# Optimization experiments

Hardware: AMD Instinct MI355X
Metric: run time of the kernel (lower is better)

## Reference

```python
import jax, jax.numpy as jnp
import numpy as np

K = 128
HEADS = 8
B = 4
T = 2048


def setup_inputs() -> dict:
    key = jax.random.key(0)
    ks = jax.random.split(key, 6)
    x = jax.random.normal(ks[0], (B, T, K), dtype=jnp.float32)
    s = 1.0 / np.sqrt(K)
    # torch nn.Linear weights are (out_features, in_features)
    Wq = jax.random.uniform(ks[1], (HEADS * K, K), dtype=jnp.float32, minval=-s, maxval=s)
    Wk = jax.random.uniform(ks[2], (HEADS * K, K), dtype=jnp.float32, minval=-s, maxval=s)
    Wv = jax.random.uniform(ks[3], (HEADS * K, K), dtype=jnp.float32, minval=-s, maxval=s)
    su = 1.0 / np.sqrt(HEADS * K)
    Wu = jax.random.uniform(ks[4], (K, HEADS * K), dtype=jnp.float32, minval=-su, maxval=su)
    bu = jax.random.uniform(ks[5], (K,), dtype=jnp.float32, minval=-su, maxval=su)
    return {"x": x, "Wq": Wq, "Wk": Wk, "Wv": Wv, "Wu": Wu, "bu": bu}


def reference(x, Wq, Wk, Wv, Wu, bu):
    b, t, k = x.shape
    h = HEADS
    # project: Linear(k, k*h) then view(b,t,h,k); weight reshaped to (h, k_out, k_in)
    q = jnp.einsum('btk,hdk->bhtd', x, Wq.reshape(h, k, k))
    kk = jnp.einsum('btk,hdk->bhtd', x, Wk.reshape(h, k, k))
    v = jnp.einsum('btk,hdk->bhtd', x, Wv.reshape(h, k, k))
    scale = jnp.asarray(k, x.dtype) ** 0.25
    q = q / scale
    kk = kk / scale
    dot = jnp.einsum('bhtd,bhsd->bhts', q, kk)  # [b,h,t,t]
    att = jax.nn.softmax(dot, axis=-1)
    out = jnp.einsum('bhts,bhsd->bhtd', att, v)  # [b,h,t,k]
    out = out.transpose(0, 2, 1, 3).reshape(b, t, h * k)
    return out @ Wu.T + bu
```

## Files before the change

### kernel.cpp

```cpp
#include <hip/hip_runtime.h>
#include <cmath>

namespace {

constexpr int HEADS = 8;
constexpr int Bn = 4;
constexpr int Tn = 2048;
constexpr int Dn = 128;
constexpr float Q_PRESCALE = 0.1275174340f;

typedef _Float16 half8 __attribute__((ext_vector_type(8)));
typedef _Float16 half4 __attribute__((ext_vector_type(4)));
typedef _Float16 half2v __attribute__((ext_vector_type(2)));
typedef float f32x4 __attribute__((ext_vector_type(4)));
typedef float f32x16 __attribute__((ext_vector_type(16)));
typedef unsigned int u32;
typedef unsigned int u32x4 __attribute__((ext_vector_type(4)));

__global__ __launch_bounds__(256) void cast_kernel(
    const float* __restrict__ x, const float* __restrict__ Wq, const float* __restrict__ Wk,
    const float* __restrict__ Wv, const float* __restrict__ Wu, _Float16* __restrict__ xh,
    _Float16* __restrict__ WH) {
  const int idx = blockIdx.x * 256 + threadIdx.x;
  const size_t base = (size_t)idx * 8;
  const float* src;
  _Float16* dst;
  if (base < 1048576) {
    src = x + base;
    dst = xh + base;
  } else {
    const size_t r = base - 1048576;
    const int s = (int)(r >> 17);
    src = ((s == 0) ? Wq : (s == 1) ? Wk : (s == 2) ? Wv : Wu) + (r & 131071);
    dst = WH + r;
  }
  const float4 a = *reinterpret_cast<const float4*>(src);
  const float4 b = *reinterpret_cast<const float4*>(src + 4);
  half8 h;
  h[0] = (_Float16)a.x; h[1] = (_Float16)a.y; h[2] = (_Float16)a.z; h[3] = (_Float16)a.w;
  h[4] = (_Float16)b.x; h[5] = (_Float16)b.y; h[6] = (_Float16)b.z; h[7] = (_Float16)b.w;
  *reinterpret_cast<half8*>(dst) = h;
}

__global__ __launch_bounds__(256, 4) void proj_kernel(const _Float16* __restrict__ xh,
                                                      const _Float16* __restrict__ WH,
                                                      _Float16* __restrict__ Qh,
                                                      _Float16* __restrict__ Kh,
                                                      _Float16* __restrict__ Vt) {
  __shared__ _Float16 sB[128 * 136];
  const int tid = threadIdx.x;
  const int w = tid >> 6, lane = tid & 63, quad = lane >> 4, l16 = lane & 15;
  const int m0 = blockIdx.x * 128;
  const int n0 = blockIdx.y * 128;

#pragma unroll
  for (int it = 0; it < 8; ++it) {
    const int fid = tid + it * 256;
    const int r = fid >> 4, g = fid & 15;
    const half8 v = *reinterpret_cast<const half8*>(WH + (size_t)(n0 + r) * 128 + g * 8);
    const int p = g ^ (r & 15);
    *reinterpret_cast<half8*>(sB + r * 128 + p * 8) = v;
  }

  half8 af[2][4];
  const _Float16* xp = xh + (size_t)(m0 + w * 32 + l16) * 128 + quad * 8;
#pragma unroll
  for (int mt = 0; mt < 2; ++mt)
#pragma unroll
    for (int kk = 0; kk < 4; ++kk)
      af[mt][kk] = *reinterpret_cast<const half8*>(xp + mt * 16 * 128 + kk * 32);

  __syncthreads();

  f32x4 acc[2][8];
#pragma unroll
  for (int mt = 0; mt < 2; ++mt)
#pragma unroll
    for (int nt = 0; nt < 8; ++nt) acc[mt][nt] = (f32x4){0.f, 0.f, 0.f, 0.f};

#pragma unroll
  for (int kk = 0; kk < 4; ++kk)
#pragma unroll
    for (int nt = 0; nt < 8; ++nt) {
      const int r = nt * 16 + l16;
      const int p = (kk * 4 + quad) ^ l16;
      const half8 bf = *reinterpret_cast<const half8*>(sB + r * 128 + p * 8);
      acc[0][nt] = __builtin_amdgcn_mfma_f32_16x16x32_f16(af[0][kk], bf, acc[0][nt], 0, 0, 0);
      acc[1][nt] = __builtin_amdgcn_mfma_f32_16x16x32_f16(af[1][kk], bf, acc[1][nt], 0, 0, 0);
    }

  const int sel = n0 >> 10;
  const int h = (n0 >> 7) & 7;
  const int b = m0 >> 11;
  const int t0b = m0 & 2047;
  const int bh = b * HEADS + h;
  const float scale = (sel == 0) ? Q_PRESCALE : 1.0f;

  __syncthreads();

  if (sel < 2) {
#pragma unroll
    for (int mt = 0; mt < 2; ++mt)
#pragma unroll
      for (int nt = 0; nt < 8; ++nt)
#pragma unroll
        for (int r = 0; r < 4; ++r)
          sB[(w * 32 + mt * 16 + quad * 4 + r) * 136 + nt * 16 + l16] =
              (_Float16)(acc[mt][nt][r] * scale);
  } else {
#pragma unroll
    for (int mt = 0; mt < 2; ++mt)
#pragma unroll
      for (int nt = 0; nt < 8; ++nt)
#pragma unroll
        for (int r = 0; r < 4; ++r)
          sB[(nt * 16 + l16) * 136 + w * 32 + mt * 16 + quad * 4 + r] = (_Float16)acc[mt][nt][r];
  }
  __syncthreads();

  _Float16* dstbase;
  size_t rstride;
  if (sel == 0) {
    dstbase = Qh + ((size_t)bh * Tn + t0b) * Dn;
    rstride = Dn;
  } else if (sel == 1) {
    dstbase = Kh + ((size_t)bh * Tn + t0b) * Dn;
    rstride = Dn;
  } else {
    dstbase = Vt + ((size_t)bh * Dn) * Tn + t0b;
    rstride = Tn;
  }
#pragma unroll
  for (int it = 0; it < 8; ++it) {
    const int fid = tid + it * 256;
    const int r = fid >> 4, g = fid & 15;
    const half8 v = *reinterpret_cast<const half8*>(sB + r * 136 + g * 8);
    *reinterpret_cast<half8*>(dstbase + (size_t)r * rstride + g * 8) = v;
  }
}

__global__ __launch_bounds__(256, 1) void flash_kernel(const _Float16* __restrict__ Qh,
                                                       const _Float16* __restrict__ Kh,
                                                       const _Float16* __restrict__ Vt,
                                                       _Float16* __restrict__ Obh) {
  __shared__ _Float16 sAll[40960];

  const int tid = threadIdx.x;
  const int w = tid >> 6;
  const int lane = tid & 63;
  const int l31 = lane & 31;
  const int h = lane >> 5;
  const int qt = blockIdx.x;
  const int bh = blockIdx.y;
  constexpr int NT = Tn / 64;

  half8 qf[2][8];
#pragma unroll
  for (int qb = 0; qb < 2; ++qb) {
    const _Float16* Qp =
        Qh + ((size_t)bh * Tn + qt * 256 + w * 64 + qb * 32 + l31) * Dn + h * 8;
#pragma unroll
    for (int ds = 0; ds < 8; ++ds) qf[qb][ds] = *reinterpret_cast<const half8*>(Qp + ds * 16);
  }

  const _Float16* Kp = Kh + (size_t)bh * Tn * Dn;
  const _Float16* Vp = Vt + (size_t)bh * Dn * Tn;

  f32x16 o[4][2];
#pragma unroll
  for (int db = 0; db < 4; ++db)
#pragma unroll
    for (int qb = 0; qb < 2; ++qb) o[db][qb] = (f32x16)(0.f);
  float lsum[2] = {0.f, 0.f};

  half8 kreg[4], vreg[4];
  const int kr = tid >> 4, kg = tid & 15;
  const int vr = tid >> 3, vg = tid & 7;
  const int vG = (vg >> 1) * 2;
  const int vO = (vg & 1) * 4;

#pragma unroll
  for (int it = 0; it < 4; ++it) {
    kreg[it] = *reinterpret_cast<const half8*>(Kp + (size_t)(kr + it * 16) * Dn + kg * 8);
    vreg[it] = *reinterpret_cast<const half8*>(Vp + (size_t)(vr + it * 32) * Tn + vg * 8);
  }
  {
    _Float16* sK0 = sAll;
    _Float16* sV0 = sAll + 16384;
#pragma unroll
    for (int it = 0; it < 4; ++it) {
      const int r = kr + it * 16;
      const int p = kg ^ (r & 15);
      *reinterpret_cast<half8*>(sK0 + r * 128 + p * 8) = kreg[it];
      const int rv = vr + it * 32;
      const int sw = (rv & 7) ^ ((rv >> 1) & 4);
      const half8 v = vreg[it];
      half4 lo, hi;
      lo[0] = v[0]; lo[1] = v[1]; lo[2] = v[2]; lo[3] = v[3];
      hi[0] = v[4]; hi[1] = v[5]; hi[2] = v[6]; hi[3] = v[7];
      *reinterpret_cast<half4*>(sV0 + rv * 64 + ((vG ^ sw) * 8) + vO) = lo;
      *reinterpret_cast<half4*>(sV0 + rv * 64 + (((vG + 1) ^ sw) * 8) + vO) = hi;
    }
  }
#pragma unroll
  for (int it = 0; it < 4; ++it) {
    kreg[it] = *reinterpret_cast<const half8*>(Kp + (size_t)(64 + kr + it * 16) * Dn + kg * 8);
    vreg[it] = *reinterpret_cast<const half8*>(Vp + (size_t)(vr + it * 32) * Tn + 64 + vg * 8);
  }
  __syncthreads();

  f32x16 scA[2][2], scB[2][2];
#pragma unroll
  for (int a = 0; a < 2; ++a)
#pragma unroll
    for (int b2 = 0; b2 < 2; ++b2) scA[a][b2] = (f32x16)(0.f);
#pragma unroll
  for (int ds = 0; ds < 8; ++ds) {
    const int p = (ds * 2 + h) ^ (l31 & 15);
    const half8 kf0 = *reinterpret_cast<const half8*>(sAll + l31 * 128 + p * 8);
    const half8 kf1 = *reinterpret_cast<const half8*>(sAll + (32 + l31) * 128 + p * 8);
    scA[0][0] = __builtin_amdgcn_mfma_f32_32x32x16_f16(kf0, qf[0][ds], scA[0][0], 0, 0, 0);
    scA[0][1] = __builtin_amdgcn_mfma_f32_32x32x16_f16(kf1, qf[0][ds], scA[0][1], 0, 0, 0);
    scA[1][0] = __builtin_amdgcn_mfma_f32_32x32x16_f16(kf0, qf[1][ds], scA[1][0], 0, 0, 0);
    scA[1][1] = __builtin_amdgcn_mfma_f32_32x32x16_f16(kf1, qf[1][ds], scA[1][1], 0, 0, 0);
  }

  auto step = [&](int t, f32x16 (&sc)[2][2], f32x16 (&sn)[2][2]) {
    _Float16* sKn = sAll + ((t + 1) & 1) * 8192;
    _Float16* sVc = sAll + 16384 + (t % 3) * 8192;
    _Float16* sVn = sAll + 16384 + ((t + 1) % 3) * 8192;

    if (t + 1 < NT) {
#pragma unroll
      for (int it = 0; it < 4; ++it) {
        const int r = kr + it * 16;
        const int p = kg ^ (r & 15);
        *reinterpret_cast<half8*>(sKn + r * 128 + p * 8) = kreg[it];
        const int rv = vr + it * 32;
        const int sw = (rv & 7) ^ ((rv >> 1) & 4);
        const half8 v = vreg[it];
        half4 lo, hi;
        lo[0] = v[0]; lo[1] = v[1]; lo[2] = v[2]; lo[3] = v[3];
        hi[0] = v[4]; hi[1] = v[5]; hi[2] = v[6]; hi[3] = v[7];
        *reinterpret_cast<half4*>(sVn + rv * 64 + ((vG ^ sw) * 8) + vO) = lo;
        *reinterpret_cast<half4*>(sVn + rv * 64 + (((vG + 1) ^ sw) * 8) + vO) = hi;
      }
    }
    __syncthreads();
    if (t + 2 < NT) {
      const _Float16* knext = Kp + (size_t)(t + 2) * 64 * Dn;
      const _Float16* vnext = Vp + (t + 2) * 64;
#pragma unroll
      for (int it = 0; it < 4; ++it) {
        kreg[it] = *reinterpret_cast<const half8*>(knext + (size_t)(kr + it * 16) * Dn + kg * 8);
        vreg[it] = *reinterpret_cast<const half8*>(vnext + (size_t)(vr + it * 32) * Tn + vg * 8);
      }
    }

    if (t + 1 < NT) {
#pragma unroll
      for (int a = 0; a < 2; ++a)
#pragma unroll
        for (int b2 = 0; b2 < 2; ++b2) sn[a][b2] = (f32x16)(0.f);
    }

    half8 bfr[2][4];
#pragma unroll
    for (int i = 0; i < 4; ++i) {
      const int qb = i & 1, kb = i >> 1;
      {
        u32 pk[8];
        float part = 0.f;
#pragma unroll
        for (int j = 0; j < 8; ++j) {
          const float e0 = __builtin_amdgcn_exp2f(sc[qb][kb][2 * j]);
          const float e1 = __builtin_amdgcn_exp2f(sc[qb][kb][2 * j + 1]);
          part += e0 + e1;
          half2v hp = {(_Float16)e0, (_Float16)e1};
          pk[j] = __builtin_bit_cast(u32, hp);
        }
        lsum[qb] += part;
        u32x4 beven = {pk[0], pk[1], pk[2], pk[3]};
        u32x4 bodd = {pk[4], pk[5], pk[6], pk[7]};
        bfr[qb][kb * 2] = __builtin_bit_cast(half8, beven);
        bfr[qb][kb * 2 + 1] = __builtin_bit_cast(half8, bodd);
      }
      if (t + 1 < NT) {
#pragma unroll
        for (int dd = 0; dd < 2; ++dd) {
          const int ds = 2 * i + dd;
          const int p = (ds * 2 + h) ^ (l31 & 15);
          const half8 kf0 = *reinterpret_cast<const half8*>(sKn + l31 * 128 + p * 8);
          const half8 kf1 = *reinterpret_cast<const half8*>(sKn + (32 + l31) * 128 + p * 8);
          sn[0][0] = __builtin_amdgcn_mfma_f32_32x32x16_f16(kf0, qf[0][ds], sn[0][0], 0, 0, 0);
          sn[0][1] = __builtin_amdgcn_mfma_f32_32x32x16_f16(kf1, qf[0][ds], sn[0][1], 0, 0, 0);
          sn[1][0] = __builtin_amdgcn_mfma_f32_32x32x16_f16(kf0, qf[1][ds], sn[1][0], 0, 0, 0);
          sn[1][1] = __builtin_amdgcn_mfma_f32_32x32x16_f16(kf1, qf[1][ds], sn[1][1], 0, 0, 0);
        }
      }
      if (i >= 1) {
        const int kb16 = i - 1;
#pragma unroll
        for (int db = 0; db < 4; ++db) {
          const int r = db * 32 + l31;
          const int pv = (kb16 * 2 + h) ^ ((r & 7) ^ ((r >> 1) & 4));
          const half8 vf = *reinterpret_cast<const half8*>(sVc + r * 64 + pv * 8);
          o[db][0] = __builtin_amdgcn_mfma_f32_32x32x16_f16(vf, bfr[0][kb16], o[db][0], 0, 0, 0);
          o[db][1] = __builtin_amdgcn_mfma_f32_32x32x16_f16(vf, bfr[1][kb16], o[db][1], 0, 0, 0);
        }
      }
    }
    {
      const int kb16 = 3;
#pragma unroll
      for (int db = 0; db < 4; ++db) {
        const int r = db * 32 + l31;
        const int pv = (kb16 * 2 + h) ^ ((r & 7) ^ ((r >> 1) & 4));
        const half8 vf = *reinterpret_cast<const half8*>(sVc + r * 64 + pv * 8);
        o[db][0] = __builtin_amdgcn_mfma_f32_32x32x16_f16(vf, bfr[0][kb16], o[db][0], 0, 0, 0);
        o[db][1] = __builtin_amdgcn_mfma_f32_32x32x16_f16(vf, bfr[1][kb16], o[db][1], 0, 0, 0);
      }
    }
  };

  for (int st = 0; st < NT; st += 2) {
    step(st, scA, scB);
    step(st + 1, scB, scA);
  }

  float inv[2];
#pragma unroll
  for (int qb = 0; qb < 2; ++qb) {
    float ls = lsum[qb];
    ls += __shfl_xor(ls, 32);
    inv[qb] = 1.0f / ls;
  }

  __syncthreads();
  _Float16* const sO = sAll + w * 8192;

#pragma unroll
  for (int qb = 0; qb < 2; ++qb) {
    const int qrow = qb * 32 + l31;
#pragma unroll
    for (int db = 0; db < 4; ++db)
#pragma unroll
      for (int grp = 0; grp < 4; ++grp) {
        const int d0 = db * 32 + grp * 8 + h * 4;
        half4 hv;
#pragma unroll
        for (int i = 0; i < 4; ++i) hv[i] = (_Float16)(o[db][qb][grp * 4 + i] * inv[qb]);
        const int idx = qrow * 128 + (((d0 >> 3) ^ (qrow & 15)) << 3) + (d0 & 7);
        *reinterpret_cast<half4*>(sO + idx) = hv;
      }
  }
  const int b = bh >> 3, hh = bh & 7;
#pragma unroll
  for (int it = 0; it < 16; ++it) {
    const int idx = lane + it * 64;
    const int row = idx >> 4, g = idx & 15;
    const half8 v = *reinterpret_cast<const half8*>(sO + row * 128 + ((g ^ (row & 15)) << 3));
    const size_t t = (size_t)(b * Tn + qt * 256 + w * 64 + row);
    *reinterpret_cast<half8*>(Obh + t * (HEADS * Dn) + hh * 128 + g * 8) = v;
  }
}

__global__ __launch_bounds__(256, 2) void outproj_kernel(const _Float16* __restrict__ Obh,
                                                         const _Float16* __restrict__ Wuh,
                                                         const float* __restrict__ bu,
                                                         float* __restrict__ out) {
  __shared__ float sR[4 * 32 * 128];
  const int tid = threadIdx.x;
  const int w = tid >> 6, lane = tid & 63, quad = lane >> 4, l16 = lane & 15;
  const int r0 = blockIdx.x * 32;

  f32x4 acc[2][8];
#pragma unroll
  for (int mt = 0; mt < 2; ++mt)
#pragma unroll
    for (int nt = 0; nt < 8; ++nt) acc[mt][nt] = (f32x4){0.f, 0.f, 0.f, 0.f};

  const _Float16* ap = Obh + (size_t)(r0 + l16) * 1024 + w * 256 + quad * 8;
  const _Float16* bp = Wuh + (size_t)l16 * 1024 + w * 256 + quad * 8;

#pragma unroll
  for (int kk = 0; kk < 8; ++kk) {
    const half8 a0 = *reinterpret_cast<const half8*>(ap + kk * 32);
    const half8 a1 = *reinterpret_cast<const half8*>(ap + 16 * 1024 + kk * 32);
#pragma unroll
    for (int nt = 0; nt < 8; ++nt) {
      const half8 bf = *reinterpret_cast<const half8*>(bp + (size_t)nt * 16 * 1024 + kk * 32);
      acc[0][nt] = __builtin_amdgcn_mfma_f32_16x16x32_f16(a0, bf, acc[0][nt], 0, 0, 0);
      acc[1][nt] = __builtin_amdgcn_mfma_f32_16x16x32_f16(a1, bf, acc[1][nt], 0, 0, 0);
    }
  }

#pragma unroll
  for (int mt = 0; mt < 2; ++mt)
#pragma unroll
    for (int nt = 0; nt < 8; ++nt)
#pragma unroll
      for (int r = 0; r < 4; ++r)
        sR[w * 4096 + (mt * 16 + quad * 4 + r) * 128 + nt * 16 + l16] = acc[mt][nt][r];
  __syncthreads();

#pragma unroll
  for (int it = 0; it < 16; ++it) {
    const int idx = tid + it * 256;
    const int row = idx >> 7, col = idx & 127;
    const float v = sR[idx] + sR[4096 + idx] + sR[8192 + idx] + sR[12288 + idx] + bu[col];
    out[(size_t)(r0 + row) * Dn + col] = v;
  }
}

}

extern "C" void kernel_launch(void* const* d_in, const int* in_sizes, int n_in, void* d_out,
                              int out_size, void* d_ws, size_t ws_size, hipStream_t stream) {
  (void)in_sizes; (void)n_in; (void)out_size; (void)ws_size;
  const float* x = (const float*)d_in[0];
  const float* Wq = (const float*)d_in[1];
  const float* Wk = (const float*)d_in[2];
  const float* Wv = (const float*)d_in[3];
  const float* Wu = (const float*)d_in[4];
  const float* bu = (const float*)d_in[5];
  float* out = (float*)d_out;

  constexpr size_t NE = (size_t)Bn * HEADS * Tn * Dn;
  char* ws = (char*)d_ws;
  _Float16* xh = (_Float16*)ws;
  _Float16* WH = (_Float16*)(ws + 2097152);
  _Float16* Qh = (_Float16*)(ws + 4194304);
  _Float16* Kh = (_Float16*)(ws + 4194304 + NE * 2);
  _Float16* Vt = (_Float16*)(ws + 4194304 + NE * 4);
  _Float16* Obh = (_Float16*)(ws + 4194304 + NE * 6);
  _Float16* Wuh = WH + 393216;

  cast_kernel<<<dim3(768), 256, 0, stream>>>(x, Wq, Wk, Wv, Wu, xh, WH);
  proj_kernel<<<dim3(64, 24), 256, 0, stream>>>(xh, WH, Qh, Kh, Vt);
  flash_kernel<<<dim3(8, 32), 256, 0, stream>>>(Qh, Kh, Vt, Obh);
  outproj_kernel<<<dim3(256), 256, 0, stream>>>(Obh, Wuh, bu, out);
}
```

Baseline: 167.9 us.

## Split flash attention work across 8 waves with 32 query rows each

The flash kernel now launches 512 threads per block, and each wave owns 32 query rows instead of 64. Per-thread Q fragments, accumulators, score tiles and K/V staging registers are halved, and the cooperative K/V loads are spread across twice as many threads. The aim is to cut register pressure so more waves can hide memory and MFMA latency, at the cost of each block's shared K/V tiles being reused by fewer rows per wave and more waves contending at every barrier. Shared memory stays at 80KB per block, so fitting two blocks per CU depends on the LDS budget.

```diff
diff --git a/kernel.cpp b/kernel.cpp
--- a/kernel.cpp
+++ b/kernel.cpp
@@ -139,7 +139,7 @@
   }
 }
 
-__global__ __launch_bounds__(256, 1) void flash_kernel(const _Float16* __restrict__ Qh,
+__global__ __launch_bounds__(512, 2) void flash_kernel(const _Float16* __restrict__ Qh,
                                                        const _Float16* __restrict__ Kh,
                                                        const _Float16* __restrict__ Vt,
                                                        _Float16* __restrict__ Obh) {
@@ -154,45 +154,41 @@
   const int bh = blockIdx.y;
   constexpr int NT = Tn / 64;
 
-  half8 qf[2][8];
-#pragma unroll
-  for (int qb = 0; qb < 2; ++qb) {
-    const _Float16* Qp =
-        Qh + ((size_t)bh * Tn + qt * 256 + w * 64 + qb * 32 + l31) * Dn + h * 8;
-#pragma unroll
-    for (int ds = 0; ds < 8; ++ds) qf[qb][ds] = *reinterpret_cast<const half8*>(Qp + ds * 16);
+  half8 qf[8];
+  {
+    const _Float16* Qp = Qh + ((size_t)bh * Tn + qt * 256 + w * 32 + l31) * Dn + h * 8;
+#pragma unroll
+    for (int ds = 0; ds < 8; ++ds) qf[ds] = *reinterpret_cast<const half8*>(Qp + ds * 16);
   }
 
   const _Float16* Kp = Kh + (size_t)bh * Tn * Dn;
   const _Float16* Vp = Vt + (size_t)bh * Dn * Tn;
 
-  f32x16 o[4][2];
-#pragma unroll
-  for (int db = 0; db < 4; ++db)
-#pragma unroll
-    for (int qb = 0; qb < 2; ++qb) o[db][qb] = (f32x16)(0.f);
-  float lsum[2] = {0.f, 0.f};
-
-  half8 kreg[4], vreg[4];
+  f32x16 o[4];
+#pragma unroll
+  for (int db = 0; db < 4; ++db) o[db] = (f32x16)(0.f);
+  float lsum = 0.f;
+
+  half8 kreg[2], vreg[2];
   const int kr = tid >> 4, kg = tid & 15;
   const int vr = tid >> 3, vg = tid & 7;
   const int vG = (vg >> 1) * 2;
   const int vO = (vg & 1) * 4;
 
 #pragma unroll
-  for (int it = 0; it < 4; ++it) {
-    kreg[it] = *reinterpret_cast<const half8*>(Kp + (size_t)(kr + it * 16) * Dn + kg * 8);
-    vreg[it] = *reinterpret_cast<const half8*>(Vp + (size_t)(vr + it * 32) * Tn + vg * 8);
+  for (int it = 0; it < 2; ++it) {
+    kreg[it] = *reinterpret_cast<const half8*>(Kp + (size_t)(kr + it * 32) * Dn + kg * 8);
+    vreg[it] = *reinterpret_cast<const half8*>(Vp + (size_t)(vr + it * 64) * Tn + vg * 8);
   }
   {
     _Float16* sK0 = sAll;
     _Float16* sV0 = sAll + 16384;
 #pragma unroll
-    for (int it = 0; it < 4; ++it) {
-      const int r = kr + it * 16;
+    for (int it = 0; it < 2; ++it) {
+      const int r = kr + it * 32;
       const int p = kg ^ (r & 15);
       *reinterpret_cast<half8*>(sK0 + r * 128 + p * 8) = kreg[it];
-      const int rv = vr + it * 32;
+      const int rv = vr + it * 64;
       const int sw = (rv & 7) ^ ((rv >> 1) & 4);
       const half8 v = vreg[it];
       half4 lo, hi;
@@ -203,40 +199,36 @@
     }
   }
 #pragma unroll
-  for (int it = 0; it < 4; ++it) {
-    kreg[it] = *reinterpret_cast<const half8*>(Kp + (size_t)(64 + kr + it * 16) * Dn + kg * 8);
-    vreg[it] = *reinterpret_cast<const half8*>(Vp + (size_t)(vr + it * 32) * Tn + 64 + vg * 8);
-  }
-  __syncthreads();
-
-  f32x16 scA[2][2], scB[2][2];
-#pragma unroll
-  for (int a = 0; a < 2; ++a)
-#pragma unroll
-    for (int b2 = 0; b2 < 2; ++b2) scA[a][b2] = (f32x16)(0.f);
+  for (int it = 0; it < 2; ++it) {
+    kreg[it] = *reinterpret_cast<const half8*>(Kp + (size_t)(64 + kr + it * 32) * Dn + kg * 8);
+    vreg[it] = *reinterpret_cast<const half8*>(Vp + (size_t)(vr + it * 64) * Tn + 64 + vg * 8);
+  }
+  __syncthreads();
+
+  f32x16 scA[2], scB[2];
+  scA[0] = (f32x16)(0.f);
+  scA[1] = (f32x16)(0.f);
 #pragma unroll
   for (int ds = 0; ds < 8; ++ds) {
     const int p = (ds * 2 + h) ^ (l31 & 15);
     const half8 kf0 = *reinterpret_cast<const half8*>(sAll + l31 * 128 + p * 8);
     const half8 kf1 = *reinterpret_cast<const half8*>(sAll + (32 + l31) * 128 + p * 8);
-    scA[0][0] = __builtin_amdgcn_mfma_f32_32x32x16_f16(kf0, qf[0][ds], scA[0][0], 0, 0, 0);
-    scA[0][1] = __builtin_amdgcn_mfma_f32_32x32x16_f16(kf1, qf[0][ds], scA[0][1], 0, 0, 0);
-    scA[1][0] = __builtin_amdgcn_mfma_f32_32x32x16_f16(kf0, qf[1][ds], scA[1][0], 0, 0, 0);
-    scA[1][1] = __builtin_amdgcn_mfma_f32_32x32x16_f16(kf1, qf[1][ds], scA[1][1], 0, 0, 0);
-  }
-
-  auto step = [&](int t, f32x16 (&sc)[2][2], f32x16 (&sn)[2][2]) {
+    scA[0] = __builtin_amdgcn_mfma_f32_32x32x16_f16(kf0, qf[ds], scA[0], 0, 0, 0);
+    scA[1] = __builtin_amdgcn_mfma_f32_32x32x16_f16(kf1, qf[ds], scA[1], 0, 0, 0);
+  }
+
+  auto step = [&](int t, f32x16 (&sc)[2], f32x16 (&sn)[2]) {
     _Float16* sKn = sAll + ((t + 1) & 1) * 8192;
     _Float16* sVc = sAll + 16384 + (t % 3) * 8192;
     _Float16* sVn = sAll + 16384 + ((t + 1) % 3) * 8192;
 
     if (t + 1 < NT) {
 #pragma unroll
-      for (int it = 0; it < 4; ++it) {
-        const int r = kr + it * 16;
+      for (int it = 0; it < 2; ++it) {
+        const int r = kr + it * 32;
         const int p = kg ^ (r & 15);
         *reinterpret_cast<half8*>(sKn + r * 128 + p * 8) = kreg[it];
-        const int rv = vr + it * 32;
+        const int rv = vr + it * 64;
         const int sw = (rv & 7) ^ ((rv >> 1) & 4);
         const half8 v = vreg[it];
         half4 lo, hi;
@@ -251,74 +243,72 @@
       const _Float16* knext = Kp + (size_t)(t + 2) * 64 * Dn;
       const _Float16* vnext = Vp + (t + 2) * 64;
 #pragma unroll
-      for (int it = 0; it < 4; ++it) {
-        kreg[it] = *reinterpret_cast<const half8*>(knext + (size_t)(kr + it * 16) * Dn + kg * 8);
-        vreg[it] = *reinterpret_cast<const half8*>(vnext + (size_t)(vr + it * 32) * Tn + vg * 8);
+      for (int it = 0; it < 2; ++it) {
+        kreg[it] = *reinterpret_cast<const half8*>(knext + (size_t)(kr + it * 32) * Dn + kg * 8);
+        vreg[it] = *reinterpret_cast<const half8*>(vnext + (size_t)(vr + it * 64) * Tn + vg * 8);
       }
     }
 
     if (t + 1 < NT) {
-#pragma unroll
-      for (int a = 0; a < 2; ++a)
-#pragma unroll
-        for (int b2 = 0; b2 < 2; ++b2) sn[a][b2] = (f32x16)(0.f);
-    }
-
-    half8 bfr[2][4];
-#pragma unroll
-    for (int i = 0; i < 4; ++i) {
-      const int qb = i & 1, kb = i >> 1;
+      sn[0] = (f32x16)(0.f);
+      sn[1] = (f32x16)(0.f);
+    }
+
+    half8 bfr[4];
+#pragma unroll
+    for (int i = 0; i < 2; ++i) {
+      const int kb = i;
       {
         u32 pk[8];
         float part = 0.f;
 #pragma unroll
         for (int j = 0; j < 8; ++j) {
-          const float e0 = __builtin_amdgcn_exp2f(sc[qb][kb][2 * j]);
-          const float e1 = __builtin_amdgcn_exp2f(sc[qb][kb][2 * j + 1]);
+          const float e0 = __builtin_amdgcn_exp2f(sc[kb][2 * j]);
+          const float e1 = __builtin_amdgcn_exp2f(sc[kb][2 * j + 1]);
           part += e0 + e1;
           half2v hp = {(_Float16)e0, (_Float16)e1};
           pk[j] = __builtin_bit_cast(u32, hp);
         }
-        lsum[qb] += part;
+        lsum += part;
         u32x4 beven = {pk[0], pk[1], pk[2], pk[3]};
         u32x4 bodd = {pk[4], pk[5], pk[6], pk[7]};
-        bfr[qb][kb * 2] = __builtin_bit_cast(half8, beven);
-        bfr[qb][kb * 2 + 1] = __builtin_bit_cast(half8, bodd);
+        bfr[kb * 2] = __builtin_bit_cast(half8, beven);
+        bfr[kb * 2 + 1] = __builtin_bit_cast(half8, bodd);
       }
       if (t + 1 < NT) {
 #pragma unroll
-        for (int dd = 0; dd < 2; ++dd) {
-          const int ds = 2 * i + dd;
+        for (int dd = 0; dd < 4; ++dd) {
+          const int ds = 4 * i + dd;
           const int p = (ds * 2 + h) ^ (l31 & 15);
           const half8 kf0 = *reinterpret_cast<const half8*>(sKn + l31 * 128 + p * 8);
           const half8 kf1 = *reinterpret_cast<const half8*>(sKn + (32 + l31) * 128 + p * 8);
-          sn[0][0] = __builtin_amdgcn_mfma_f32_32x32x16_f16(kf0, qf[0][ds], sn[0][0], 0, 0, 0);
-          sn[0][1] = __builtin_amdgcn_mfma_f32_32x32x16_f16(kf1, qf[0][ds], sn[0][1], 0, 0, 0);
-          sn[1][0] = __builtin_amdgcn_mfma_f32_32x32x16_f16(kf0, qf[1][ds], sn[1][0], 0, 0, 0);
-          sn[1][1] = __builtin_amdgcn_mfma_f32_32x32x16_f16(kf1, qf[1][ds], sn[1][1], 0, 0, 0);
+          sn[0] = __builtin_amdgcn_mfma_f32_32x32x16_f16(kf0, qf[ds], sn[0], 0, 0, 0);
+          sn[1] = __builtin_amdgcn_mfma_f32_32x32x16_f16(kf1, qf[ds], sn[1], 0, 0, 0);
         }
       }
       if (i >= 1) {
-        const int kb16 = i - 1;
-#pragma unroll
-        for (int db = 0; db < 4; ++db) {
-          const int r = db * 32 + l31;
-          const int pv = (kb16 * 2 + h) ^ ((r & 7) ^ ((r >> 1) & 4));
-          const half8 vf = *reinterpret_cast<const half8*>(sVc + r * 64 + pv * 8);
-          o[db][0] = __builtin_amdgcn_mfma_f32_32x32x16_f16(vf, bfr[0][kb16], o[db][0], 0, 0, 0);
-          o[db][1] = __builtin_amdgcn_mfma_f32_32x32x16_f16(vf, bfr[1][kb16], o[db][1], 0, 0, 0);
+#pragma unroll
+        for (int kk = 0; kk < 2; ++kk) {
+          const int kb16 = kk;
+#pragma unroll
+          for (int db = 0; db < 4; ++db) {
+            const int r = db * 32 + l31;
+            const int pv = (kb16 * 2 + h) ^ ((r & 7) ^ ((r >> 1) & 4));
+            const half8 vf = *reinterpret_cast<const half8*>(sVc + r * 64 + pv * 8);
+            o[db] = __builtin_amdgcn_mfma_f32_32x32x16_f16(vf, bfr[kb16], o[db], 0, 0, 0);
+          }
         }
       }
     }
-    {
-      const int kb16 = 3;
+#pragma unroll
+    for (int kk = 2; kk < 4; ++kk) {
+      const int kb16 = kk;
 #pragma unroll
       for (int db = 0; db < 4; ++db) {
         const int r = db * 32 + l31;
         const int pv = (kb16 * 2 + h) ^ ((r & 7) ^ ((r >> 1) & 4));
         const half8 vf = *reinterpret_cast<const half8*>(sVc + r * 64 + pv * 8);
-        o[db][0] = __builtin_amdgcn_mfma_f32_32x32x16_f16(vf, bfr[0][kb16], o[db][0], 0, 0, 0);
-        o[db][1] = __builtin_amdgcn_mfma_f32_32x32x16_f16(vf, bfr[1][kb16], o[db][1], 0, 0, 0);
+        o[db] = __builtin_amdgcn_mfma_f32_32x32x16_f16(vf, bfr[kb16], o[db], 0, 0, 0);
       }
     }
   };
@@ -328,20 +318,18 @@
     step(st + 1, scB, scA);
   }
 
-  float inv[2];
-#pragma unroll
-  for (int qb = 0; qb < 2; ++qb) {
-    float ls = lsum[qb];
+  float inv;
+  {
+    float ls = lsum;
     ls += __shfl_xor(ls, 32);
-    inv[qb] = 1.0f / ls;
-  }
-
-  __syncthreads();
-  _Float16* const sO = sAll + w * 8192;
-
-#pragma unroll
-  for (int qb = 0; qb < 2; ++qb) {
-    const int qrow = qb * 32 + l31;
+    inv = 1.0f / ls;
+  }
+
+  __syncthreads();
+  _Float16* const sO = sAll + w * 4096;
+
+  {
+    const int qrow = l31;
 #pragma unroll
     for (int db = 0; db < 4; ++db)
 #pragma unroll
@@ -349,18 +337,18 @@
         const int d0 = db * 32 + grp * 8 + h * 4;
         half4 hv;
 #pragma unroll
-        for (int i = 0; i < 4; ++i) hv[i] = (_Float16)(o[db][qb][grp * 4 + i] * inv[qb]);
+        for (int i = 0; i < 4; ++i) hv[i] = (_Float16)(o[db][grp * 4 + i] * inv);
         const int idx = qrow * 128 + (((d0 >> 3) ^ (qrow & 15)) << 3) + (d0 & 7);
         *reinterpret_cast<half4*>(sO + idx) = hv;
       }
   }
   const int b = bh >> 3, hh = bh & 7;
 #pragma unroll
-  for (int it = 0; it < 16; ++it) {
+  for (int it = 0; it < 8; ++it) {
     const int idx = lane + it * 64;
     const int row = idx >> 4, g = idx & 15;
     const half8 v = *reinterpret_cast<const half8*>(sO + row * 128 + ((g ^ (row & 15)) << 3));
-    const size_t t = (size_t)(b * Tn + qt * 256 + w * 64 + row);
+    const size_t t = (size_t)(b * Tn + qt * 256 + w * 32 + row);
     *reinterpret_cast<half8*>(Obh + t * (HEADS * Dn) + hh * 128 + g * 8) = v;
   }
 }
@@ -438,6 +426,6 @@
 
   cast_kernel<<<dim3(768), 256, 0, stream>>>(x, Wq, Wk, Wv, Wu, xh, WH);
   proj_kernel<<<dim3(64, 24), 256, 0, stream>>>(xh, WH, Qh, Kh, Vt);
-  flash_kernel<<<dim3(8, 32), 256, 0, stream>>>(Qh, Kh, Vt, Obh);
+  flash_kernel<<<dim3(8, 32), 512, 0, stream>>>(Qh, Kh, Vt, Obh);
   outproj_kernel<<<dim3(256), 256, 0, stream>>>(Obh, Wuh, bu, out);
 }
```

After: 170.1 us. About the same (+1.3%).
